# Kernel optimization log

Hardware: AMD Instinct MI355X
Metric: run time of the kernel (lower is better)

## Reference

```python
import jax, jax.numpy as jnp
import numpy as np

N = 50000
E = 1600000
IN = 128
HID = 32
HEADS = 4
SLOPE = 0.2   # GATConv default negative_slope
EPS = 1e-5    # BatchNorm eps


def setup_inputs() -> dict:
    key = jax.random.key(0)
    ks = jax.random.split(key, 16)
    inp = {}
    inp["x"] = jax.random.normal(ks[0], (N, IN), dtype=jnp.float32)
    inp["edge_index"] = jax.random.randint(ks[1], (2, E), 0, N, dtype=jnp.int32)
    def p(k, shape, s=0.1):
        return jax.random.normal(k, shape, dtype=jnp.float32) * s
    # layer dims: (in_ch, out_ch_per_head, heads, concat)
    dims = [(IN, HID, HEADS, True), (HID * HEADS, HID, HEADS, True), (HID * HEADS, HID, 1, False)]
    i = 2
    for li, (ic, oc, h, concat) in enumerate(dims):
        inp[f"W{li}"] = p(ks[i], (ic, h * oc)); i += 1
        inp[f"as{li}"] = p(ks[i], (h, oc)); i += 1
        inp[f"ad{li}"] = p(ks[i], (h, oc)); i += 1
        bn_dim = h * oc if concat else oc
        inp[f"b{li}"] = jnp.zeros((bn_dim,), jnp.float32)
        inp[f"g{li}"] = jnp.ones((bn_dim,), jnp.float32)
        inp[f"be{li}"] = jnp.zeros((bn_dim,), jnp.float32)
    inp["cw1"] = p(ks[i], (HID, HID // 2)); i += 1
    inp["cb1"] = jnp.zeros((HID // 2,), jnp.float32)
    inp["cw2"] = p(ks[i], (HID // 2, 2)); i += 1
    inp["cb2"] = jnp.zeros((2,), jnp.float32)
    return inp


def _gat_layer(h, src, dst, W, a_s, a_d, b, heads, oc, concat):
    # PyG GATConv: x -> [N,H,C]; alpha = softmax_dst(leaky_relu(a_s.x_src + a_d.x_dst))
    n = h.shape[0]
    x = (h @ W).reshape(n, heads, oc)                 # [N,H,C]
    e_s = (x * a_s).sum(-1)                            # [N,H]
    e_d = (x * a_d).sum(-1)                            # [N,H]
    e = jax.nn.leaky_relu(e_s[src] + e_d[dst], SLOPE)  # [Etot,H]
    m = jax.ops.segment_max(e, dst, num_segments=n)    # segment softmax over dst
    ex = jnp.exp(e - m[dst])
    den = jax.ops.segment_sum(ex, dst, num_segments=n)
    alpha = ex / (den[dst] + 1e-16)                    # [Etot,H]
    out = jax.ops.segment_sum(x[src] * alpha[:, :, None], dst, num_segments=n)  # [N,H,C]
    out = out.reshape(n, heads * oc) if concat else out.mean(1)
    return out + b


def _bn(x, g, be):
    mu = x.mean(0)
    var = x.var(0)  # biased, as torch BN uses for normalization
    return g * (x - mu) * jax.lax.rsqrt(var + EPS) + be


def reference(x, edge_index, W0, as0, ad0, b0, g0, be0, W1, as1, ad1, b1, g1, be1,
              W2, as2, ad2, b2, g2, be2, cw1, cb1, cw2, cb2):
    n = x.shape[0]
    loops = jnp.arange(n, dtype=edge_index.dtype)      # add_self_loops=True default
    src = jnp.concatenate([edge_index[0], loops])
    dst = jnp.concatenate([edge_index[1], loops])
    layers = [(W0, as0, ad0, b0, g0, be0, HEADS, HID, True),
              (W1, as1, ad1, b1, g1, be1, HEADS, HID, True),
              (W2, as2, ad2, b2, g2, be2, 1, HID, False)]
    h = x
    for (W, a_s, a_d, b, g, be, heads, oc, concat) in layers:
        h = _gat_layer(h, src, dst, W, a_s, a_d, b, heads, oc, concat)
        h = jax.nn.elu(_bn(h, g, be))
    h = jax.nn.elu(h @ cw1 + cb1)
    return h @ cw2 + cb2
```

## Files before the change

kernel.cpp:

```cpp
#include <hip/hip_runtime.h>

static constexpr float SLOPE = 0.2f;
static constexpr float BN_EPS = 1e-5f;

static inline int cdiv(long long a, long long b) { return (int)((a + b - 1) / b); }

typedef __attribute__((ext_vector_type(8))) short short8;
typedef __attribute__((ext_vector_type(4))) float f32x4;

__device__ __forceinline__ unsigned short f2bf(float f) {
  unsigned u = __float_as_uint(f);
  u += 0x7fff + ((u >> 16) & 1);
  return (unsigned short)(u >> 16);
}
__device__ __forceinline__ float bf2f(unsigned short h) {
  return __uint_as_float((unsigned)h << 16);
}

static constexpr int EPB = 8192;
static constexpr int BCAP = 12288;

__global__ void prep_hist(const int* __restrict__ ei, int* __restrict__ counts,
                          const float* __restrict__ W0, const float* __restrict__ W1,
                          const float* __restrict__ W2,
                          unsigned short* __restrict__ Wt0, unsigned short* __restrict__ Wt1,
                          unsigned short* __restrict__ Wt2,
                          float* __restrict__ sums0, float* __restrict__ sums1,
                          float* __restrict__ sums2,
                          int E, int NBLK, int NB) {
  const int tid = threadIdx.x;
  const int blk = blockIdx.x;
  if (blk < NBLK) {
    __shared__ int cnt[256];
    cnt[tid] = 0;
    __syncthreads();
    const int i0 = blk * EPB;
    const int i1 = min(E, i0 + EPB);
    for (int i = i0 + tid; i < i1; i += 256) atomicAdd(&cnt[ei[E + i] >> 8], 1);
    __syncthreads();
    if (tid < NB) counts[tid * NBLK + blk] = cnt[tid];
    return;
  }
  const int b = blk - NBLK;
  if (b < 64) {
    int o = b * 256 + tid;
    int j = o >> 7, k = o & 127;
    Wt0[o] = f2bf(W0[k * 128 + j]);
  } else if (b < 128) {
    int o = (b - 64) * 256 + tid;
    int j = o >> 7, k = o & 127;
    Wt1[o] = f2bf(W1[k * 128 + j]);
  } else if (b < 144) {
    int o = (b - 128) * 256 + tid;
    int j = o >> 7, k = o & 127;
    Wt2[o] = f2bf(W2[k * 32 + j]);
  } else {
    sums0[tid] = 0.f;
    sums1[tid] = 0.f;
    if (tid < 64) sums2[tid] = 0.f;
  }
}

__global__ void csr_scan2(const int* __restrict__ counts, int* __restrict__ offsets, int m) {
  __shared__ int wtot[16];
  const int tid = threadIdx.x;
  const int lane = tid & 63, wv = tid >> 6;
  const int CH = (m + 1023) >> 10;
  const int lo = min(m, tid * CH);
  const int hi = min(m, lo + CH);
  int sum = 0;
  for (int i = lo; i < hi; ++i) sum += counts[i];
  int x = sum;
#pragma unroll
  for (int off = 1; off < 64; off <<= 1) {
    int y = __shfl_up(x, off);
    if (lane >= off) x += y;
  }
  if (lane == 63) wtot[wv] = x;
  __syncthreads();
  int add = 0;
  for (int w = 0; w < wv; ++w) add += wtot[w];
  int run = x - sum + add;
  for (int i = lo; i < hi; ++i) { offsets[i] = run; run += counts[i]; }
  if (hi == m) offsets[m] = run;
}

__global__ __launch_bounds__(256) void csr_part(const int* __restrict__ ei,
                                                const int* __restrict__ offsets,
                                                unsigned* __restrict__ ebuf,
                                                int E, int NBLK, int NB) {
  __shared__ unsigned stage[EPB];
  __shared__ int cnt[256], sstart[256], cur[256], goff[256];
  __shared__ int wtot[4];
  const int tid = threadIdx.x;
  const int blk = blockIdx.x;
  const int lane = tid & 63, wv = tid >> 6;
  cnt[tid] = 0;
  if (tid < NB) goff[tid] = offsets[tid * NBLK + blk];
  __syncthreads();
  const int i0 = blk * EPB;
  const int i1 = min(E, i0 + EPB);
  for (int i = i0 + tid; i < i1; i += 256) atomicAdd(&cnt[ei[E + i] >> 8], 1);
  __syncthreads();
  int v = cnt[tid];
  int x = v;
#pragma unroll
  for (int off = 1; off < 64; off <<= 1) {
    int y = __shfl_up(x, off);
    if (lane >= off) x += y;
  }
  if (lane == 63) wtot[wv] = x;
  __syncthreads();
  int add = 0;
  for (int w = 0; w < wv; ++w) add += wtot[w];
  int excl = x - v + add;
  sstart[tid] = excl;
  cur[tid] = excl;
  __syncthreads();
  for (int i = i0 + tid; i < i1; i += 256) {
    int s = ei[i], d = ei[E + i];
    int p = atomicAdd(&cur[d >> 8], 1);
    stage[p] = ((unsigned)s << 8) | (unsigned)(d & 255);
  }
  __syncthreads();
  for (int b = wv; b < NB; b += 4) {
    const int ls = sstart[b], le = cur[b];
    const int gbase = goff[b];
    for (int e = ls + lane; e < le; e += 64) ebuf[gbase + (e - ls)] = stage[e];
  }
}

__global__ __launch_bounds__(256) void csr_bucket(const unsigned* __restrict__ ebuf,
                                                  const int* __restrict__ offsets,
                                                  int* __restrict__ row_start,
                                                  int* __restrict__ csr_src,
                                                  int n, int E, int NBLK, int NB) {
  __shared__ unsigned stage[BCAP];
  __shared__ int deg[256], cur[256];
  __shared__ int wtot[4];
  const int b = blockIdx.x;
  const int base = b << 8;
  const int nn = min(256, n - base);
  const int estart = offsets[b * NBLK];
  const int eend = (b + 1 < NB) ? offsets[(b + 1) * NBLK] : E;
  const int gstart = estart + base;
  const int tid = threadIdx.x;
  const int lane = tid & 63, wv = tid >> 6;
  deg[tid] = (tid < nn) ? 1 : 0;
  __syncthreads();
  for (int j = estart + tid; j < eend; j += 256) atomicAdd(&deg[ebuf[j] & 255u], 1);
  __syncthreads();
  int v = deg[tid];
  int x = v;
#pragma unroll
  for (int off = 1; off < 64; off <<= 1) {
    int y = __shfl_up(x, off);
    if (lane >= off) x += y;
  }
  if (lane == 63) wtot[wv] = x;
  __syncthreads();
  int add = 0;
  for (int w = 0; w < wv; ++w) add += wtot[w];
  int excl = x - v + add;
  cur[tid] = excl;
  if (tid < nn) row_start[base + tid] = gstart + excl;
  if (b == 0 && tid == 0) row_start[n] = E + n;
  __syncthreads();
  if (tid < nn) {
    int p = atomicAdd(&cur[tid], 1);
    if (p < BCAP) stage[p] = (unsigned)(base + tid);
    else csr_src[gstart + p] = base + tid;
  }
  for (int j = estart + tid; j < eend; j += 256) {
    unsigned pk = ebuf[j];
    int p = atomicAdd(&cur[pk & 255u], 1);
    if (p < BCAP) stage[p] = pk >> 8;
    else csr_src[gstart + p] = (int)(pk >> 8);
  }
  __syncthreads();
  const int tot = min(eend - estart + nn, BCAP);
  for (int e = tid; e < tot; e += 256) csr_src[gstart + e] = (int)stage[e];
}

template<int IC, int OC, int H, bool BN, bool AF32>
__global__ void gemm_mfma(const unsigned short* __restrict__ Act,
                          const float* __restrict__ Axf,
                          const unsigned short* __restrict__ Wt,
                          const float* __restrict__ a_s, const float* __restrict__ a_d,
                          const float* __restrict__ bnsums, const float* __restrict__ g,
                          const float* __restrict__ be,
                          unsigned short* __restrict__ Pb, float* __restrict__ es,
                          float* __restrict__ ed, int n) {
  constexpr int NF = OC / 16;
  __shared__ float s_sc[IC], s_sf[IC];
  const int tid = threadIdx.x;
  if (BN) {
    const float inv_n = 1.f / (float)n;
    for (int c = tid; c < IC; c += 256) {
      float mu = bnsums[c] * inv_n;
      float var = bnsums[IC + c] * inv_n - mu * mu;
      float s = g[c] * rsqrtf(var + BN_EPS);
      s_sc[c] = s;
      s_sf[c] = be[c] - mu * s;
    }
    __syncthreads();
  }
  const int lane = tid & 63;
  const int l15 = lane & 15;
  const int lk = lane >> 4;
  const int node0 = blockIdx.x * 64 + (tid >> 6) * 16;
  const int arow = node0 + l15;
  const int ar = AF32 ? min(arow, n - 1) : arow;

  f32x4 acc[NF];
#pragma unroll
  for (int cb = 0; cb < NF; ++cb) acc[cb] = (f32x4){0.f, 0.f, 0.f, 0.f};

#pragma unroll
  for (int kc = 0; kc < IC / 32; ++kc) {
    const int kbase = kc * 32 + lk * 8;
    short8 a;
    if (AF32) {
      float4 u0 = *(const float4*)(Axf + (size_t)ar * IC + kbase);
      float4 u1 = *(const float4*)(Axf + (size_t)ar * IC + kbase + 4);
      a[0] = (short)f2bf(u0.x); a[1] = (short)f2bf(u0.y);
      a[2] = (short)f2bf(u0.z); a[3] = (short)f2bf(u0.w);
      a[4] = (short)f2bf(u1.x); a[5] = (short)f2bf(u1.y);
      a[6] = (short)f2bf(u1.z); a[7] = (short)f2bf(u1.w);
    } else {
      a = *(const short8*)(Act + (size_t)ar * IC + kbase);
    }
    if (BN) {
      short8 ta;
#pragma unroll
      for (int i = 0; i < 8; ++i) {
        float v = bf2f((unsigned short)a[i]);
        float y = fmaf(v, s_sc[kbase + i], s_sf[kbase + i]);
        y = (y > 0.f) ? y : (__expf(y) - 1.f);
        ta[i] = (short)f2bf(y);
      }
      a = ta;
    }
#pragma unroll
    for (int cb = 0; cb < NF; ++cb) {
      short8 b = *(const short8*)(Wt + (size_t)(cb * 16 + l15) * IC + kbase);
      acc[cb] = __builtin_amdgcn_mfma_f32_16x16x32_bf16(a, b, acc[cb], 0, 0, 0);
    }
  }

  float esum[4] = {0.f, 0.f, 0.f, 0.f}, edum[4] = {0.f, 0.f, 0.f, 0.f};
#pragma unroll
  for (int cb = 0; cb < NF; ++cb) {
    const int j = cb * 16 + l15;
    const float asv = a_s[j];
    const float adv = a_d[j];
#pragma unroll
    for (int i = 0; i < 4; ++i) {
      float p = acc[cb][i];
      int node = node0 + lk * 4 + i;
      if (node < n) Pb[(size_t)node * OC + j] = f2bf(p);
      float ps = p * asv, pd = p * adv;
#pragma unroll
      for (int mm = 1; mm <= 8; mm <<= 1) {
        ps += __shfl_xor(ps, mm);
        pd += __shfl_xor(pd, mm);
      }
      esum[i] += ps;
      edum[i] += pd;
    }
    if (cb & 1) {
      const int h = cb >> 1;
#pragma unroll
      for (int i = 0; i < 4; ++i) {
        int node = node0 + lk * 4 + i;
        if (l15 == 0 && node < n) {
          es[node * H + h] = esum[i];
          ed[node * H + h] = edum[i];
        }
        esum[i] = 0.f;
        edum[i] = 0.f;
      }
    }
  }
}

template<int H, int C>
__global__ void node_agg(const int* __restrict__ row_start, const int* __restrict__ csr_src,
                         const float* __restrict__ es, const float* __restrict__ ed,
                         const unsigned short* __restrict__ Pb, unsigned short* __restrict__ Ob,
                         int n) {
  constexpr int HC = H * C;
  constexpr int TPN = HC / 8;
  const int tid = threadIdx.x;
  const int t = tid % TPN;
  const int node = blockIdx.x * (256 / TPN) + tid / TPN;
  if (node >= n) return;
  const int h = (t * 8) / C;
  const int e0 = row_start[node];
  const int e1 = row_start[node + 1];
  const float edd = ed[node * H + h];
  const uint4* P4 = (const uint4*)Pb;
  float a0 = 0.f, a1 = 0.f, a2 = 0.f, a3 = 0.f;
  float a4 = 0.f, a5 = 0.f, a6 = 0.f, a7 = 0.f;
  float den = 0.f;
  int s0 = csr_src[e0];
  int s1 = (e0 + 1 < e1) ? csr_src[e0 + 1] : s0;
  int s2 = (e0 + 2 < e1) ? csr_src[e0 + 2] : s0;
  int s3 = (e0 + 3 < e1) ? csr_src[e0 + 3] : s0;
  for (int j = e0; j < e1; j += 4) {
    const int nj = j + 4;
    int t0 = (nj     < e1) ? csr_src[nj]     : s0;
    int t1 = (nj + 1 < e1) ? csr_src[nj + 1] : s0;
    int t2 = (nj + 2 < e1) ? csr_src[nj + 2] : s0;
    int t3 = (nj + 3 < e1) ? csr_src[nj + 3] : s0;
    float x0 = es[s0 * H + h], x1 = es[s1 * H + h];
    float x2 = es[s2 * H + h], x3 = es[s3 * H + h];
    uint4 p0 = P4[(size_t)s0 * TPN + t];
    uint4 p1 = P4[(size_t)s1 * TPN + t];
    uint4 p2 = P4[(size_t)s2 * TPN + t];
    uint4 p3 = P4[(size_t)s3 * TPN + t];
    x0 += edd; x0 = fmaxf(x0, SLOPE * x0);
    x1 += edd; x1 = fmaxf(x1, SLOPE * x1);
    x2 += edd; x2 = fmaxf(x2, SLOPE * x2);
    x3 += edd; x3 = fmaxf(x3, SLOPE * x3);
    float w0 = __expf(x0);
    float w1 = (j + 1 < e1) ? __expf(x1) : 0.f;
    float w2 = (j + 2 < e1) ? __expf(x2) : 0.f;
    float w3 = (j + 3 < e1) ? __expf(x3) : 0.f;
    den += (w0 + w1) + (w2 + w3);
    a0 = fmaf(w0, __uint_as_float(p0.x << 16), a0);
    a1 = fmaf(w0, __uint_as_float(p0.x & 0xffff0000u), a1);
    a2 = fmaf(w0, __uint_as_float(p0.y << 16), a2);
    a3 = fmaf(w0, __uint_as_float(p0.y & 0xffff0000u), a3);
    a4 = fmaf(w0, __uint_as_float(p0.z << 16), a4);
    a5 = fmaf(w0, __uint_as_float(p0.z & 0xffff0000u), a5);
    a6 = fmaf(w0, __uint_as_float(p0.w << 16), a6);
    a7 = fmaf(w0, __uint_as_float(p0.w & 0xffff0000u), a7);
    a0 = fmaf(w1, __uint_as_float(p1.x << 16), a0);
    a1 = fmaf(w1, __uint_as_float(p1.x & 0xffff0000u), a1);
    a2 = fmaf(w1, __uint_as_float(p1.y << 16), a2);
    a3 = fmaf(w1, __uint_as_float(p1.y & 0xffff0000u), a3);
    a4 = fmaf(w1, __uint_as_float(p1.z << 16), a4);
    a5 = fmaf(w1, __uint_as_float(p1.z & 0xffff0000u), a5);
    a6 = fmaf(w1, __uint_as_float(p1.w << 16), a6);
    a7 = fmaf(w1, __uint_as_float(p1.w & 0xffff0000u), a7);
    a0 = fmaf(w2, __uint_as_float(p2.x << 16), a0);
    a1 = fmaf(w2, __uint_as_float(p2.x & 0xffff0000u), a1);
    a2 = fmaf(w2, __uint_as_float(p2.y << 16), a2);
    a3 = fmaf(w2, __uint_as_float(p2.y & 0xffff0000u), a3);
    a4 = fmaf(w2, __uint_as_float(p2.z << 16), a4);
    a5 = fmaf(w2, __uint_as_float(p2.z & 0xffff0000u), a5);
    a6 = fmaf(w2, __uint_as_float(p2.w << 16), a6);
    a7 = fmaf(w2, __uint_as_float(p2.w & 0xffff0000u), a7);
    a0 = fmaf(w3, __uint_as_float(p3.x << 16), a0);
    a1 = fmaf(w3, __uint_as_float(p3.x & 0xffff0000u), a1);
    a2 = fmaf(w3, __uint_as_float(p3.y << 16), a2);
    a3 = fmaf(w3, __uint_as_float(p3.y & 0xffff0000u), a3);
    a4 = fmaf(w3, __uint_as_float(p3.z << 16), a4);
    a5 = fmaf(w3, __uint_as_float(p3.z & 0xffff0000u), a5);
    a6 = fmaf(w3, __uint_as_float(p3.w << 16), a6);
    a7 = fmaf(w3, __uint_as_float(p3.w & 0xffff0000u), a7);
    s0 = t0; s1 = t1; s2 = t2; s3 = t3;
  }
  float inv = 1.f / (den + 1e-16f);
  uint4 o;
  o.x = (unsigned)f2bf(a0 * inv) | ((unsigned)f2bf(a1 * inv) << 16);
  o.y = (unsigned)f2bf(a2 * inv) | ((unsigned)f2bf(a3 * inv) << 16);
  o.z = (unsigned)f2bf(a4 * inv) | ((unsigned)f2bf(a5 * inv) << 16);
  o.w = (unsigned)f2bf(a6 * inv) | ((unsigned)f2bf(a7 * inv) << 16);
  *(uint4*)(Ob + (size_t)node * HC + t * 8) = o;
}

template<int C>
__global__ void bn_stats2(const unsigned short* __restrict__ X, float* __restrict__ sums,
                          int n) {
  constexpr int TPR = C / 4;
  constexpr int RPB = 256 / TPR;
  __shared__ float ls[2 * C];
  const int tid = threadIdx.x;
  for (int i = tid; i < 2 * C; i += 256) ls[i] = 0.f;
  __syncthreads();
  const int c4 = (tid % TPR) * 4;
  const int rb = tid / TPR;
  float s0 = 0.f, s1 = 0.f, s2 = 0.f, s3 = 0.f;
  float q0 = 0.f, q1 = 0.f, q2 = 0.f, q3 = 0.f;
  for (int r = blockIdx.x * RPB + rb; r < n; r += gridDim.x * RPB) {
    uint2 v = *(const uint2*)(X + (size_t)r * C + c4);
    float f0 = __uint_as_float(v.x << 16);
    float f1 = __uint_as_float(v.x & 0xffff0000u);
    float f2 = __uint_as_float(v.y << 16);
    float f3 = __uint_as_float(v.y & 0xffff0000u);
    s0 += f0; q0 = fmaf(f0, f0, q0);
    s1 += f1; q1 = fmaf(f1, f1, q1);
    s2 += f2; q2 = fmaf(f2, f2, q2);
    s3 += f3; q3 = fmaf(f3, f3, q3);
  }
  atomicAdd(&ls[c4 + 0], s0);
  atomicAdd(&ls[c4 + 1], s1);
  atomicAdd(&ls[c4 + 2], s2);
  atomicAdd(&ls[c4 + 3], s3);
  atomicAdd(&ls[C + c4 + 0], q0);
  atomicAdd(&ls[C + c4 + 1], q1);
  atomicAdd(&ls[C + c4 + 2], q2);
  atomicAdd(&ls[C + c4 + 3], q3);
  __syncthreads();
  for (int i = tid; i < 2 * C; i += 256) unsafeAtomicAdd(&sums[i], ls[i]);
}

__global__ void mlp_head(const unsigned short* __restrict__ Hf, const float* __restrict__ bnsums,
                         const float* __restrict__ g, const float* __restrict__ be,
                         const float* __restrict__ cw1, const float* __restrict__ cb1,
                         const float* __restrict__ cw2, const float* __restrict__ cb2,
                         float* __restrict__ out, int n) {
  __shared__ float w1[32 * 16];
  __shared__ float b1[16];
  __shared__ float w2[16 * 2];
  __shared__ float b2[2];
  __shared__ float sc[32], sf[32];
  int tid = threadIdx.x;
  for (int i = tid; i < 32 * 16; i += blockDim.x) w1[i] = cw1[i];
  if (tid < 16) b1[tid] = cb1[tid];
  if (tid < 32) w2[tid] = cw2[tid];
  if (tid < 2) b2[tid] = cb2[tid];
  if (tid < 32) {
    float inv_n = 1.f / (float)n;
    float mu = bnsums[tid] * inv_n;
    float var = bnsums[32 + tid] * inv_n - mu * mu;
    float s = g[tid] * rsqrtf(var + BN_EPS);
    sc[tid] = s;
    sf[tid] = be[tid] - mu * s;
  }
  __syncthreads();
  int node = blockIdx.x * blockDim.x + tid;
  if (node >= n) return;
  float x[32];
  const uint4* xp = (const uint4*)(Hf + (size_t)node * 32);
#pragma unroll
  for (int q = 0; q < 4; ++q) {
    uint4 v = xp[q];
    unsigned pr[4] = {v.x, v.y, v.z, v.w};
#pragma unroll
    for (int u = 0; u < 4; ++u) {
      int c = q * 8 + u * 2;
      float va = __uint_as_float(pr[u] << 16);
      float vb = __uint_as_float(pr[u] & 0xffff0000u);
      float ya = fmaf(va, sc[c], sf[c]);
      float yb = fmaf(vb, sc[c + 1], sf[c + 1]);
      x[c] = (ya > 0.f) ? ya : (__expf(ya) - 1.f);
      x[c + 1] = (yb > 0.f) ? yb : (__expf(yb) - 1.f);
    }
  }
  float o0 = b2[0], o1 = b2[1];
#pragma unroll
  for (int j = 0; j < 16; ++j) {
    float acc = b1[j];
#pragma unroll
    for (int k = 0; k < 32; ++k) acc = fmaf(x[k], w1[k * 16 + j], acc);
    acc = (acc > 0.f) ? acc : (__expf(acc) - 1.f);
    o0 = fmaf(acc, w2[j * 2 + 0], o0);
    o1 = fmaf(acc, w2[j * 2 + 1], o1);
  }
  out[(size_t)node * 2 + 0] = o0;
  out[(size_t)node * 2 + 1] = o1;
}

extern "C" void kernel_launch(void* const* d_in, const int* in_sizes, int n_in,
                              void* d_out, int out_size, void* d_ws, size_t ws_size,
                              hipStream_t stream) {
  const float* x   = (const float*)d_in[0];
  const int*   ei  = (const int*)d_in[1];
  const float* W0  = (const float*)d_in[2];
  const float* as0 = (const float*)d_in[3];
  const float* ad0 = (const float*)d_in[4];
  const float* g0  = (const float*)d_in[6];
  const float* be0 = (const float*)d_in[7];
  const float* W1  = (const float*)d_in[8];
  const float* as1 = (const float*)d_in[9];
  const float* ad1 = (const float*)d_in[10];
  const float* g1  = (const float*)d_in[12];
  const float* be1 = (const float*)d_in[13];
  const float* W2  = (const float*)d_in[14];
  const float* as2 = (const float*)d_in[15];
  const float* ad2 = (const float*)d_in[16];
  const float* g2  = (const float*)d_in[18];
  const float* be2 = (const float*)d_in[19];
  const float* cw1 = (const float*)d_in[20];
  const float* cb1 = (const float*)d_in[21];
  const float* cw2 = (const float*)d_in[22];
  const float* cb2 = (const float*)d_in[23];

  const int n = in_sizes[0] / 128;
  const int E = in_sizes[1] / 2;
  const int n64 = cdiv(n, 64) * 64;

  const int NBLK = cdiv(E, EPB);
  const int NB = cdiv(n, 256);
  const int m = NB * NBLK;

  unsigned short* Ab  = (unsigned short*)d_ws;
  unsigned short* Bb  = Ab + (size_t)n64 * 128;
  unsigned short* Pb  = Bb + (size_t)n64 * 128;
  unsigned short* Af  = Pb + (size_t)n64 * 128;
  unsigned short* Wt0 = Af + (size_t)n64 * 32;
  unsigned short* Wt1 = Wt0 + 128 * 128;
  unsigned short* Wt2 = Wt1 + 128 * 128;
  float* es    = (float*)(Wt2 + 32 * 128);
  float* ed    = es + (size_t)n * 4;
  float* sums0 = ed + (size_t)n * 4;
  float* sums1 = sums0 + 256;
  float* sums2 = sums1 + 256;
  int* counts    = (int*)(sums2 + 64);
  int* offsets   = counts + m;
  int* row_start = offsets + m + 1;
  int* csr_src   = row_start + n + 1;
  unsigned* ebuf = (unsigned*)(csr_src + E + n);

  prep_hist<<<NBLK + 145, 256, 0, stream>>>(ei, counts, W0, W1, W2, Wt0, Wt1, Wt2,
                                            sums0, sums1, sums2, E, NBLK, NB);
  csr_scan2<<<1, 1024, 0, stream>>>(counts, offsets, m);
  csr_part<<<NBLK, 256, 0, stream>>>(ei, offsets, ebuf, E, NBLK, NB);
  csr_bucket<<<NB, 256, 0, stream>>>(ebuf, offsets, row_start, csr_src, n, E, NBLK, NB);

  gemm_mfma<128, 128, 4, false, true><<<cdiv(n, 64), 256, 0, stream>>>(
      nullptr, x, Wt0, as0, ad0, nullptr, nullptr, nullptr, Pb, es, ed, n);
  node_agg<4, 32><<<cdiv(n, 16), 256, 0, stream>>>(row_start, csr_src, es, ed, Pb, Ab, n);
  bn_stats2<128><<<1024, 256, 0, stream>>>(Ab, sums0, n);

  gemm_mfma<128, 128, 4, true, false><<<cdiv(n, 64), 256, 0, stream>>>(
      Ab, nullptr, Wt1, as1, ad1, sums0, g0, be0, Pb, es, ed, n);
  node_agg<4, 32><<<cdiv(n, 16), 256, 0, stream>>>(row_start, csr_src, es, ed, Pb, Bb, n);
  bn_stats2<128><<<1024, 256, 0, stream>>>(Bb, sums1, n);

  gemm_mfma<128, 32, 1, true, false><<<cdiv(n, 64), 256, 0, stream>>>(
      Bb, nullptr, Wt2, as2, ad2, sums1, g1, be1, Pb, es, ed, n);
  node_agg<1, 32><<<cdiv(n, 64), 256, 0, stream>>>(row_start, csr_src, es, ed, Pb, Af, n);
  bn_stats2<32><<<512, 256, 0, stream>>>(Af, sums2, n);

  mlp_head<<<cdiv(n, 256), 256, 0, stream>>>(Af, sums2, g2, be2, cw1, cb1, cw2, cb2,
                                             (float*)d_out, n);
}
```

Baseline: 424.6 us.

## Fuse BatchNorm statistics into aggregation and stage GEMM output through LDS

BatchNorm sum and sum-of-squares accumulation moves from a separate bn_stats2 pass into node_agg. Each block reduces in shared memory, then atomically adds into one of 64 partial buffers, and a small finalize kernel sums the partials. This removes a full re-read of each layer's activations. The GEMM epilogue now writes bf16 results to LDS and stores them as coalesced 16-byte rows instead of scattered 2-byte stores. Costs are extra LDS atomics in the aggregation, one more tiny kernel launch per layer, and zeroing larger partial buffers at startup. Statistics are now taken from fp32 values before bf16 rounding, which changes numerics slightly.

```diff
diff --git a/kernel.cpp b/kernel.cpp
--- a/kernel.cpp
+++ b/kernel.cpp
@@ -25,8 +25,8 @@
                           const float* __restrict__ W2,
                           unsigned short* __restrict__ Wt0, unsigned short* __restrict__ Wt1,
                           unsigned short* __restrict__ Wt2,
-                          float* __restrict__ sums0, float* __restrict__ sums1,
-                          float* __restrict__ sums2,
+                          float* __restrict__ SP0, float* __restrict__ SP1,
+                          float* __restrict__ SP2,
                           int E, int NBLK, int NB) {
   const int tid = threadIdx.x;
   const int blk = blockIdx.x;
@@ -55,9 +55,12 @@
     int j = o >> 7, k = o & 127;
     Wt2[o] = f2bf(W2[k * 32 + j]);
   } else {
-    sums0[tid] = 0.f;
-    sums1[tid] = 0.f;
-    if (tid < 64) sums2[tid] = 0.f;
+    int idx = (b - 144) * 256 + tid;
+    for (int i = idx; i < 36864; i += 48 * 256) {
+      if (i < 16384) SP0[i] = 0.f;
+      else if (i < 32768) SP1[i - 16384] = 0.f;
+      else SP2[i - 32768] = 0.f;
+    }
   }
 }
 
@@ -193,6 +196,7 @@
                           float* __restrict__ ed, int n) {
   constexpr int NF = OC / 16;
   __shared__ float s_sc[IC], s_sf[IC];
+  __shared__ unsigned short s_stage[4 * 16 * OC];
   const int tid = threadIdx.x;
   if (BN) {
     const float inv_n = 1.f / (float)n;
@@ -208,7 +212,8 @@
   const int lane = tid & 63;
   const int l15 = lane & 15;
   const int lk = lane >> 4;
-  const int node0 = blockIdx.x * 64 + (tid >> 6) * 16;
+  const int wid = tid >> 6;
+  const int node0 = blockIdx.x * 64 + wid * 16;
   const int arow = node0 + l15;
   const int ar = AF32 ? min(arow, n - 1) : arow;
 
@@ -248,6 +253,7 @@
     }
   }
 
+  unsigned short* st = s_stage + wid * 16 * OC;
   float esum[4] = {0.f, 0.f, 0.f, 0.f}, edum[4] = {0.f, 0.f, 0.f, 0.f};
 #pragma unroll
   for (int cb = 0; cb < NF; ++cb) {
@@ -257,8 +263,7 @@
 #pragma unroll
     for (int i = 0; i < 4; ++i) {
       float p = acc[cb][i];
-      int node = node0 + lk * 4 + i;
-      if (node < n) Pb[(size_t)node * OC + j] = f2bf(p);
+      st[(lk * 4 + i) * OC + j] = f2bf(p);
       float ps = p * asv, pd = p * adv;
 #pragma unroll
       for (int mm = 1; mm <= 8; mm <<= 1) {
@@ -282,129 +287,128 @@
       }
     }
   }
+  for (int idx = lane; idx < 2 * OC; idx += 64) {
+    int r = idx / (OC / 8);
+    int q = idx % (OC / 8);
+    int node = node0 + r;
+    if (node < n)
+      *(uint4*)(Pb + (size_t)node * OC + q * 8) = *(const uint4*)(st + r * OC + q * 8);
+  }
 }
 
 template<int H, int C>
 __global__ void node_agg(const int* __restrict__ row_start, const int* __restrict__ csr_src,
                          const float* __restrict__ es, const float* __restrict__ ed,
                          const unsigned short* __restrict__ Pb, unsigned short* __restrict__ Ob,
-                         int n) {
+                         float* __restrict__ sums_part, int n) {
   constexpr int HC = H * C;
   constexpr int TPN = HC / 8;
-  const int tid = threadIdx.x;
+  __shared__ float ls[2 * HC];
+  const int tid = threadIdx.x;
+  for (int i = tid; i < 2 * HC; i += 256) ls[i] = 0.f;
+  __syncthreads();
   const int t = tid % TPN;
   const int node = blockIdx.x * (256 / TPN) + tid / TPN;
-  if (node >= n) return;
-  const int h = (t * 8) / C;
-  const int e0 = row_start[node];
-  const int e1 = row_start[node + 1];
-  const float edd = ed[node * H + h];
-  const uint4* P4 = (const uint4*)Pb;
-  float a0 = 0.f, a1 = 0.f, a2 = 0.f, a3 = 0.f;
-  float a4 = 0.f, a5 = 0.f, a6 = 0.f, a7 = 0.f;
-  float den = 0.f;
-  int s0 = csr_src[e0];
-  int s1 = (e0 + 1 < e1) ? csr_src[e0 + 1] : s0;
-  int s2 = (e0 + 2 < e1) ? csr_src[e0 + 2] : s0;
-  int s3 = (e0 + 3 < e1) ? csr_src[e0 + 3] : s0;
-  for (int j = e0; j < e1; j += 4) {
-    const int nj = j + 4;
-    int t0 = (nj     < e1) ? csr_src[nj]     : s0;
-    int t1 = (nj + 1 < e1) ? csr_src[nj + 1] : s0;
-    int t2 = (nj + 2 < e1) ? csr_src[nj + 2] : s0;
-    int t3 = (nj + 3 < e1) ? csr_src[nj + 3] : s0;
-    float x0 = es[s0 * H + h], x1 = es[s1 * H + h];
-    float x2 = es[s2 * H + h], x3 = es[s3 * H + h];
-    uint4 p0 = P4[(size_t)s0 * TPN + t];
-    uint4 p1 = P4[(size_t)s1 * TPN + t];
-    uint4 p2 = P4[(size_t)s2 * TPN + t];
-    uint4 p3 = P4[(size_t)s3 * TPN + t];
-    x0 += edd; x0 = fmaxf(x0, SLOPE * x0);
-    x1 += edd; x1 = fmaxf(x1, SLOPE * x1);
-    x2 += edd; x2 = fmaxf(x2, SLOPE * x2);
-    x3 += edd; x3 = fmaxf(x3, SLOPE * x3);
-    float w0 = __expf(x0);
-    float w1 = (j + 1 < e1) ? __expf(x1) : 0.f;
-    float w2 = (j + 2 < e1) ? __expf(x2) : 0.f;
-    float w3 = (j + 3 < e1) ? __expf(x3) : 0.f;
-    den += (w0 + w1) + (w2 + w3);
-    a0 = fmaf(w0, __uint_as_float(p0.x << 16), a0);
-    a1 = fmaf(w0, __uint_as_float(p0.x & 0xffff0000u), a1);
-    a2 = fmaf(w0, __uint_as_float(p0.y << 16), a2);
-    a3 = fmaf(w0, __uint_as_float(p0.y & 0xffff0000u), a3);
-    a4 = fmaf(w0, __uint_as_float(p0.z << 16), a4);
-    a5 = fmaf(w0, __uint_as_float(p0.z & 0xffff0000u), a5);
-    a6 = fmaf(w0, __uint_as_float(p0.w << 16), a6);
-    a7 = fmaf(w0, __uint_as_float(p0.w & 0xffff0000u), a7);
-    a0 = fmaf(w1, __uint_as_float(p1.x << 16), a0);
-    a1 = fmaf(w1, __uint_as_float(p1.x & 0xffff0000u), a1);
-    a2 = fmaf(w1, __uint_as_float(p1.y << 16), a2);
-    a3 = fmaf(w1, __uint_as_float(p1.y & 0xffff0000u), a3);
-    a4 = fmaf(w1, __uint_as_float(p1.z << 16), a4);
-    a5 = fmaf(w1, __uint_as_float(p1.z & 0xffff0000u), a5);
-    a6 = fmaf(w1, __uint_as_float(p1.w << 16), a6);
-    a7 = fmaf(w1, __uint_as_float(p1.w & 0xffff0000u), a7);
-    a0 = fmaf(w2, __uint_as_float(p2.x << 16), a0);
-    a1 = fmaf(w2, __uint_as_float(p2.x & 0xffff0000u), a1);
-    a2 = fmaf(w2, __uint_as_float(p2.y << 16), a2);
-    a3 = fmaf(w2, __uint_as_float(p2.y & 0xffff0000u), a3);
-    a4 = fmaf(w2, __uint_as_float(p2.z << 16), a4);
-    a5 = fmaf(w2, __uint_as_float(p2.z & 0xffff0000u), a5);
-    a6 = fmaf(w2, __uint_as_float(p2.w << 16), a6);
-    a7 = fmaf(w2, __uint_as_float(p2.w & 0xffff0000u), a7);
-    a0 = fmaf(w3, __uint_as_float(p3.x << 16), a0);
-    a1 = fmaf(w3, __uint_as_float(p3.x & 0xffff0000u), a1);
-    a2 = fmaf(w3, __uint_as_float(p3.y << 16), a2);
-    a3 = fmaf(w3, __uint_as_float(p3.y & 0xffff0000u), a3);
-    a4 = fmaf(w3, __uint_as_float(p3.z << 16), a4);
-    a5 = fmaf(w3, __uint_as_float(p3.z & 0xffff0000u), a5);
-    a6 = fmaf(w3, __uint_as_float(p3.w << 16), a6);
-    a7 = fmaf(w3, __uint_as_float(p3.w & 0xffff0000u), a7);
-    s0 = t0; s1 = t1; s2 = t2; s3 = t3;
-  }
-  float inv = 1.f / (den + 1e-16f);
-  uint4 o;
-  o.x = (unsigned)f2bf(a0 * inv) | ((unsigned)f2bf(a1 * inv) << 16);
-  o.y = (unsigned)f2bf(a2 * inv) | ((unsigned)f2bf(a3 * inv) << 16);
-  o.z = (unsigned)f2bf(a4 * inv) | ((unsigned)f2bf(a5 * inv) << 16);
-  o.w = (unsigned)f2bf(a6 * inv) | ((unsigned)f2bf(a7 * inv) << 16);
-  *(uint4*)(Ob + (size_t)node * HC + t * 8) = o;
+  if (node < n) {
+    const int h = (t * 8) / C;
+    const int e0 = row_start[node];
+    const int e1 = row_start[node + 1];
+    const float edd = ed[node * H + h];
+    const uint4* P4 = (const uint4*)Pb;
+    float a0 = 0.f, a1 = 0.f, a2 = 0.f, a3 = 0.f;
+    float a4 = 0.f, a5 = 0.f, a6 = 0.f, a7 = 0.f;
+    float den = 0.f;
+    int s0 = csr_src[e0];
+    int s1 = (e0 + 1 < e1) ? csr_src[e0 + 1] : s0;
+    int s2 = (e0 + 2 < e1) ? csr_src[e0 + 2] : s0;
+    int s3 = (e0 + 3 < e1) ? csr_src[e0 + 3] : s0;
+    for (int j = e0; j < e1; j += 4) {
+      const int nj = j + 4;
+      int t0 = (nj     < e1) ? csr_src[nj]     : s0;
+      int t1 = (nj + 1 < e1) ? csr_src[nj + 1] : s0;
+      int t2 = (nj + 2 < e1) ? csr_src[nj + 2] : s0;
+      int t3 = (nj + 3 < e1) ? csr_src[nj + 3] : s0;
+      float x0 = es[s0 * H + h], x1 = es[s1 * H + h];
+      float x2 = es[s2 * H + h], x3 = es[s3 * H + h];
+      uint4 p0 = P4[(size_t)s0 * TPN + t];
+      uint4 p1 = P4[(size_t)s1 * TPN + t];
+      uint4 p2 = P4[(size_t)s2 * TPN + t];
+      uint4 p3 = P4[(size_t)s3 * TPN + t];
+      x0 += edd; x0 = fmaxf(x0, SLOPE * x0);
+      x1 += edd; x1 = fmaxf(x1, SLOPE * x1);
+      x2 += edd; x2 = fmaxf(x2, SLOPE * x2);
+      x3 += edd; x3 = fmaxf(x3, SLOPE * x3);
+      float w0 = __expf(x0);
+      float w1 = (j + 1 < e1) ? __expf(x1) : 0.f;
+      float w2 = (j + 2 < e1) ? __expf(x2) : 0.f;
+      float w3 = (j + 3 < e1) ? __expf(x3) : 0.f;
+      den += (w0 + w1) + (w2 + w3);
+      a0 = fmaf(w0, __uint_as_float(p0.x << 16), a0);
+      a1 = fmaf(w0, __uint_as_float(p0.x & 0xffff0000u), a1);
+      a2 = fmaf(w0, __uint_as_float(p0.y << 16), a2);
+      a3 = fmaf(w0, __uint_as_float(p0.y & 0xffff0000u), a3);
+      a4 = fmaf(w0, __uint_as_float(p0.z << 16), a4);
+      a5 = fmaf(w0, __uint_as_float(p0.z & 0xffff0000u), a5);
+      a6 = fmaf(w0, __uint_as_float(p0.w << 16), a6);
+      a7 = fmaf(w0, __uint_as_float(p0.w & 0xffff0000u), a7);
+      a0 = fmaf(w1, __uint_as_float(p1.x << 16), a0);
+      a1 = fmaf(w1, __uint_as_float(p1.x & 0xffff0000u), a1);
+      a2 = fmaf(w1, __uint_as_float(p1.y << 16), a2);
+      a3 = fmaf(w1, __uint_as_float(p1.y & 0xffff0000u), a3);
+      a4 = fmaf(w1, __uint_as_float(p1.z << 16), a4);
+      a5 = fmaf(w1, __uint_as_float(p1.z & 0xffff0000u), a5);
+      a6 = fmaf(w1, __uint_as_float(p1.w << 16), a6);
+      a7 = fmaf(w1, __uint_as_float(p1.w & 0xffff0000u), a7);
+      a0 = fmaf(w2, __uint_as_float(p2.x << 16), a0);
+      a1 = fmaf(w2, __uint_as_float(p2.x & 0xffff0000u), a1);
+      a2 = fmaf(w2, __uint_as_float(p2.y << 16), a2);
+      a3 = fmaf(w2, __uint_as_float(p2.y & 0xffff0000u), a3);
+      a4 = fmaf(w2, __uint_as_float(p2.z << 16), a4);
+      a5 = fmaf(w2, __uint_as_float(p2.z & 0xffff0000u), a5);
+      a6 = fmaf(w2, __uint_as_float(p2.w << 16), a6);
+      a7 = fmaf(w2, __uint_as_float(p2.w & 0xffff0000u), a7);
+      a0 = fmaf(w3, __uint_as_float(p3.x << 16), a0);
+      a1 = fmaf(w3, __uint_as_float(p3.x & 0xffff0000u), a1);
+      a2 = fmaf(w3, __uint_as_float(p3.y << 16), a2);
+      a3 = fmaf(w3, __uint_as_float(p3.y & 0xffff0000u), a3);
+      a4 = fmaf(w3, __uint_as_float(p3.z << 16), a4);
+      a5 = fmaf(w3, __uint_as_float(p3.z & 0xffff0000u), a5);
+      a6 = fmaf(w3, __uint_as_float(p3.w << 16), a6);
+      a7 = fmaf(w3, __uint_as_float(p3.w & 0xffff0000u), a7);
+      s0 = t0; s1 = t1; s2 = t2; s3 = t3;
+    }
+    float inv = 1.f / (den + 1e-16f);
+    a0 *= inv; a1 *= inv; a2 *= inv; a3 *= inv;
+    a4 *= inv; a5 *= inv; a6 *= inv; a7 *= inv;
+    const int c0 = t * 8;
+    atomicAdd(&ls[c0 + 0], a0); atomicAdd(&ls[HC + c0 + 0], a0 * a0);
+    atomicAdd(&ls[c0 + 1], a1); atomicAdd(&ls[HC + c0 + 1], a1 * a1);
+    atomicAdd(&ls[c0 + 2], a2); atomicAdd(&ls[HC + c0 + 2], a2 * a2);
+    atomicAdd(&ls[c0 + 3], a3); atomicAdd(&ls[HC + c0 + 3], a3 * a3);
+    atomicAdd(&ls[c0 + 4], a4); atomicAdd(&ls[HC + c0 + 4], a4 * a4);
+    atomicAdd(&ls[c0 + 5], a5); atomicAdd(&ls[HC + c0 + 5], a5 * a5);
+    atomicAdd(&ls[c0 + 6], a6); atomicAdd(&ls[HC + c0 + 6], a6 * a6);
+    atomicAdd(&ls[c0 + 7], a7); atomicAdd(&ls[HC + c0 + 7], a7 * a7);
+    uint4 o;
+    o.x = (unsigned)f2bf(a0) | ((unsigned)f2bf(a1) << 16);
+    o.y = (unsigned)f2bf(a2) | ((unsigned)f2bf(a3) << 16);
+    o.z = (unsigned)f2bf(a4) | ((unsigned)f2bf(a5) << 16);
+    o.w = (unsigned)f2bf(a6) | ((unsigned)f2bf(a7) << 16);
+    *(uint4*)(Ob + (size_t)node * HC + t * 8) = o;
+  }
+  __syncthreads();
+  float* dst = sums_part + (size_t)(blockIdx.x & 63) * (2 * HC);
+  for (int i = tid; i < 2 * HC; i += 256) unsafeAtomicAdd(&dst[i], ls[i]);
 }
 
 template<int C>
-__global__ void bn_stats2(const unsigned short* __restrict__ X, float* __restrict__ sums,
-                          int n) {
-  constexpr int TPR = C / 4;
-  constexpr int RPB = 256 / TPR;
-  __shared__ float ls[2 * C];
-  const int tid = threadIdx.x;
-  for (int i = tid; i < 2 * C; i += 256) ls[i] = 0.f;
-  __syncthreads();
-  const int c4 = (tid % TPR) * 4;
-  const int rb = tid / TPR;
-  float s0 = 0.f, s1 = 0.f, s2 = 0.f, s3 = 0.f;
-  float q0 = 0.f, q1 = 0.f, q2 = 0.f, q3 = 0.f;
-  for (int r = blockIdx.x * RPB + rb; r < n; r += gridDim.x * RPB) {
-    uint2 v = *(const uint2*)(X + (size_t)r * C + c4);
-    float f0 = __uint_as_float(v.x << 16);
-    float f1 = __uint_as_float(v.x & 0xffff0000u);
-    float f2 = __uint_as_float(v.y << 16);
-    float f3 = __uint_as_float(v.y & 0xffff0000u);
-    s0 += f0; q0 = fmaf(f0, f0, q0);
-    s1 += f1; q1 = fmaf(f1, f1, q1);
-    s2 += f2; q2 = fmaf(f2, f2, q2);
-    s3 += f3; q3 = fmaf(f3, f3, q3);
-  }
-  atomicAdd(&ls[c4 + 0], s0);
-  atomicAdd(&ls[c4 + 1], s1);
-  atomicAdd(&ls[c4 + 2], s2);
-  atomicAdd(&ls[c4 + 3], s3);
-  atomicAdd(&ls[C + c4 + 0], q0);
-  atomicAdd(&ls[C + c4 + 1], q1);
-  atomicAdd(&ls[C + c4 + 2], q2);
-  atomicAdd(&ls[C + c4 + 3], q3);
-  __syncthreads();
-  for (int i = tid; i < 2 * C; i += 256) unsafeAtomicAdd(&sums[i], ls[i]);
+__global__ void finalize_bn(const float* __restrict__ part, float* __restrict__ sums) {
+  const int tid = threadIdx.x;
+  for (int c = tid; c < 2 * C; c += 256) {
+    float s = 0.f;
+    for (int k = 0; k < 64; ++k) s += part[(size_t)k * 2 * C + c];
+    sums[c] = s;
+  }
 }
 
 __global__ void mlp_head(const unsigned short* __restrict__ Hf, const float* __restrict__ bnsums,
@@ -509,32 +513,35 @@
   float* sums0 = ed + (size_t)n * 4;
   float* sums1 = sums0 + 256;
   float* sums2 = sums1 + 256;
-  int* counts    = (int*)(sums2 + 64);
+  float* SP0   = sums2 + 64;
+  float* SP1   = SP0 + 64 * 256;
+  float* SP2   = SP1 + 64 * 256;
+  int* counts    = (int*)(SP2 + 64 * 64);
   int* offsets   = counts + m;
   int* row_start = offsets + m + 1;
   int* csr_src   = row_start + n + 1;
   unsigned* ebuf = (unsigned*)(csr_src + E + n);
 
-  prep_hist<<<NBLK + 145, 256, 0, stream>>>(ei, counts, W0, W1, W2, Wt0, Wt1, Wt2,
-                                            sums0, sums1, sums2, E, NBLK, NB);
+  prep_hist<<<NBLK + 192, 256, 0, stream>>>(ei, counts, W0, W1, W2, Wt0, Wt1, Wt2,
+                                            SP0, SP1, SP2, E, NBLK, NB);
   csr_scan2<<<1, 1024, 0, stream>>>(counts, offsets, m);
   csr_part<<<NBLK, 256, 0, stream>>>(ei, offsets, ebuf, E, NBLK, NB);
   csr_bucket<<<NB, 256, 0, stream>>>(ebuf, offsets, row_start, csr_src, n, E, NBLK, NB);
 
   gemm_mfma<128, 128, 4, false, true><<<cdiv(n, 64), 256, 0, stream>>>(
       nullptr, x, Wt0, as0, ad0, nullptr, nullptr, nullptr, Pb, es, ed, n);
-  node_agg<4, 32><<<cdiv(n, 16), 256, 0, stream>>>(row_start, csr_src, es, ed, Pb, Ab, n);
-  bn_stats2<128><<<1024, 256, 0, stream>>>(Ab, sums0, n);
+  node_agg<4, 32><<<cdiv(n, 16), 256, 0, stream>>>(row_start, csr_src, es, ed, Pb, Ab, SP0, n);
+  finalize_bn<128><<<1, 256, 0, stream>>>(SP0, sums0);
 
   gemm_mfma<128, 128, 4, true, false><<<cdiv(n, 64), 256, 0, stream>>>(
       Ab, nullptr, Wt1, as1, ad1, sums0, g0, be0, Pb, es, ed, n);
-  node_agg<4, 32><<<cdiv(n, 16), 256, 0, stream>>>(row_start, csr_src, es, ed, Pb, Bb, n);
-  bn_stats2<128><<<1024, 256, 0, stream>>>(Bb, sums1, n);
+  node_agg<4, 32><<<cdiv(n, 16), 256, 0, stream>>>(row_start, csr_src, es, ed, Pb, Bb, SP1, n);
+  finalize_bn<128><<<1, 256, 0, stream>>>(SP1, sums1);
 
   gemm_mfma<128, 32, 1, true, false><<<cdiv(n, 64), 256, 0, stream>>>(
       Bb, nullptr, Wt2, as2, ad2, sums1, g1, be1, Pb, es, ed, n);
-  node_agg<1, 32><<<cdiv(n, 64), 256, 0, stream>>>(row_start, csr_src, es, ed, Pb, Af, n);
-  bn_stats2<32><<<512, 256, 0, stream>>>(Af, sums2, n);
+  node_agg<1, 32><<<cdiv(n, 64), 256, 0, stream>>>(row_start, csr_src, es, ed, Pb, Af, SP2, n);
+  finalize_bn<32><<<1, 256, 0, stream>>>(SP2, sums2);
 
   mlp_head<<<cdiv(n, 256), 256, 0, stream>>>(Af, sums2, g2, be2, cw1, cb1, cw2, cb2,
                                              (float*)d_out, n);
```

Measured after the change: 461.8 us. 8.8% more time.
